# Performance work log

Measured on AMD Instinct MI355X. Metric: run time of the kernel, lower is better.

The kernel has to match this reference:

```python
import jax, jax.numpy as jnp
import numpy as np
from jax import lax

C_EDGE, C_DVS, C_OUT = 128, 128, 128
H, W = 32, 32
MASK_SIZE = 7
THRESH, TAU, GAMA = 1.0, 0.5, 1.0  # LIFSpike defaults (ZIF surrogate)


def _window_mask(h, w, mask_size):
    half = mask_size // 2
    qx = jnp.arange(h)[:, None, None, None]
    qy = jnp.arange(w)[None, :, None, None]
    kx = jnp.arange(h)[None, None, :, None]
    ky = jnp.arange(w)[None, None, None, :]
    allowed = (jnp.abs(kx - qx) <= half) & (jnp.abs(ky - qy) <= half)
    return jnp.where(allowed, 0.0, -10000.0).reshape(h * w, h * w).astype(jnp.float32)


@jax.custom_vjp
def _spike(x):
    return (x > 0).astype(x.dtype)

def _spike_fwd(x):
    return _spike(x), x

def _spike_bwd(x, g):
    # ZIF surrogate: grad = clamp(gama - |x|, 0) / gama^2
    return (g * jnp.clip(GAMA - jnp.abs(x), 0.0, None) / (GAMA * GAMA),)

_spike.defvjp(_spike_fwd, _spike_bwd)


def _lif(x):
    # x: (B, T, C, H, W) -> spikes, scan over time
    xt = jnp.moveaxis(x, 1, 0)  # (T, B, C, H, W)

    def step(mem, inp):
        mem = mem * TAU + inp
        spk = _spike(mem - THRESH)
        mem = (1.0 - spk) * mem
        return mem, spk

    _, spikes = lax.scan(step, jnp.zeros_like(xt[0]), xt)
    return jnp.moveaxis(spikes, 0, 1)


def setup_inputs() -> dict:
    key = jax.random.key(0)
    ks = jax.random.split(key, 16)
    s = 0.05
    return {
        "edge_features": jax.random.normal(ks[0], (8, 4, C_EDGE, H, W), jnp.float32),
        "dvs_features": jax.random.normal(ks[1], (8, 4, C_DVS, H, W), jnp.float32),
        "We": jax.random.normal(ks[2], (C_OUT, C_EDGE), jnp.float32) * s,
        "be": jax.random.normal(ks[3], (C_OUT,), jnp.float32) * s,
        "Wd": jax.random.normal(ks[4], (C_OUT, C_DVS), jnp.float32) * s,
        "bd": jax.random.normal(ks[5], (C_OUT,), jnp.float32) * s,
        "Wq": jax.random.normal(ks[6], (C_OUT, C_OUT), jnp.float32) * s,
        "bq": jax.random.normal(ks[7], (C_OUT,), jnp.float32) * s,
        "Wk": jax.random.normal(ks[8], (C_OUT, C_OUT), jnp.float32) * s,
        "bk": jax.random.normal(ks[9], (C_OUT,), jnp.float32) * s,
        "Wv": jax.random.normal(ks[10], (C_OUT, C_OUT), jnp.float32) * s,
        "bv": jax.random.normal(ks[11], (C_OUT,), jnp.float32) * s,
        "Wf": jax.random.normal(ks[12], (C_OUT, C_OUT), jnp.float32) * s,
        "bf": jax.random.normal(ks[13], (C_OUT,), jnp.float32) * s,
    }


def reference(edge_features, dvs_features, We, be, Wd, bd, Wq, bq, Wk, bk, Wv, bv, Wf, bf):
    B, T, _, h, w = dvs_features.shape
    C = We.shape[0]
    N = h * w
    # 1x1 conv channel alignment (SeqToANNContainer folds B,T)
    ef = (jnp.einsum('btchw,oc->btohw', edge_features, We) + be[None, None, :, None, None]).reshape(B * T, C, h, w)
    df = (jnp.einsum('btchw,oc->btohw', dvs_features, Wd) + bd[None, None, :, None, None]).reshape(B * T, C, h, w)
    # cosine similarity over channels
    l2e = jnp.sqrt(jnp.sum(ef * ef, axis=1, keepdims=True))
    l2d = jnp.sqrt(jnp.sum(df * df, axis=1, keepdims=True))
    sim = jnp.sum((ef / (l2e + 1e-6)) * (df / (l2d + 1e-6)), axis=1, keepdims=True)
    sim = (sim + 1.0) * 0.5
    # density: softmax of edge L2 norm over spatial, scaled by N
    dens = (jax.nn.softmax(l2e.reshape(B * T, N), axis=1) * N).reshape(B * T, 1, h, w)
    ew = (ef * sim).reshape(B * T, C, N)
    dw = (df * dens).reshape(B * T, C, N)
    # conv1d k=1 Q/K/V projections
    q = jnp.einsum('oc,bcn->bon', Wq, ew) + bq[None, :, None]
    k = jnp.einsum('oc,bcn->bon', Wk, dw) + bk[None, :, None]
    v = jnp.einsum('oc,bcn->bon', Wv, dw) + bv[None, :, None]
    mask = _window_mask(h, w, MASK_SIZE)
    attn = jnp.einsum('bcq,bck->bqk', q, k) / (C ** 0.5) + mask[None]
    attn = jax.nn.softmax(attn, axis=-1)
    out = jnp.einsum('bqk,bck->bqc', attn, v)  # (BT, N, C)
    out = out.reshape(B * T, h, w, C).transpose(0, 3, 1, 2).reshape(B, T, C, h, w)
    fused = jnp.einsum('btchw,oc->btohw', out, Wf) + bf[None, None, :, None, None]
    return _lif(fused)
```

## Files before the change

kernel.cpp:

```cpp
#include <hip/hip_runtime.h>
#include <math.h>

#define CC 128
#define NN 1024
#define BTOT 32
#define CP 152
#define PSTs 40
#define CPA 136
#define CQS 36

typedef unsigned short u16;
typedef u16 u16x8 __attribute__((ext_vector_type(8)));
typedef u16 u16x4 __attribute__((ext_vector_type(4)));
typedef __bf16 bf16x8 __attribute__((ext_vector_type(8)));
typedef float f32x4 __attribute__((ext_vector_type(4)));

__device__ __forceinline__ u16 f2b(float f) {
    unsigned int u = __float_as_uint(f);
    u += 0x7FFFu + ((u >> 16) & 1u);
    return (u16)(u >> 16);
}
__device__ __forceinline__ float b2f(u16 u) {
    return __uint_as_float(((unsigned int)u) << 16);
}

__device__ __forceinline__ void loadB(const u16* brow, int g, bf16x8 bfr[4]) {
#pragma unroll
    for (int kk = 0; kk < 4; ++kk)
        bfr[kk] = *(const bf16x8*)(brow + kk * 32 + g * 8);
}
__device__ __forceinline__ bf16x8 ldA(const u16* __restrict__ WB, int ot, int kk, int l) {
    return *(const bf16x8*)(WB + ((size_t)(ot * 4 + kk) * 64 + l) * 8);
}

__global__ __launch_bounds__(128) void k_comp(
    const float* __restrict__ Wq, const float* __restrict__ Wk,
    const float* __restrict__ Wv, const float* __restrict__ We,
    const float* __restrict__ Wd, const float* __restrict__ be,
    const float* __restrict__ bd,
    float* __restrict__ Wcomp, float* __restrict__ cvec)
{
    const int mat = blockIdx.y, o = blockIdx.x, c = threadIdx.x;
    const float* A = (mat == 0) ? Wq : (mat == 1) ? Wk : Wv;
    const float* B = (mat == 0) ? We : Wd;
    const float* bv = (mat == 0) ? be : bd;
    float acc = 0.f;
    for (int m = 0; m < CC; ++m) acc += A[o * CC + m] * B[m * CC + c];
    Wcomp[(size_t)mat * 16384 + o * CC + c] = acc;
    if (c == 0) {
        float bacc = 0.f;
        for (int m = 0; m < CC; ++m) bacc += A[o * CC + m] * bv[m];
        cvec[mat * CC + o] = bacc;
    }
}

__global__ __launch_bounds__(256) void k_wcvt(
    const float* __restrict__ W0, const float* __restrict__ W1,
    const float* __restrict__ W2, const float* __restrict__ W3,
    const float* __restrict__ W4, const float* __restrict__ W5,
    u16* __restrict__ out)
{
    const int gid = blockIdx.x * 256 + threadIdx.x;
    const int wi = gid >> 11, rem = gid & 2047;
    const float* W = (wi == 0) ? W0 : (wi == 1) ? W1 : (wi == 2) ? W2
                   : (wi == 3) ? W3 : (wi == 4) ? W4 : W5;
    const int ot = rem >> 8, kk = (rem >> 6) & 3, l = rem & 63;
    const int row = ot * 16 + (l & 15), col = kk * 32 + (l >> 4) * 8;
    float4 a = *(const float4*)(W + row * CC + col);
    float4 b = *(const float4*)(W + row * CC + col + 4);
    u16x8 u;
    u[0] = f2b(a.x); u[1] = f2b(a.y); u[2] = f2b(a.z); u[3] = f2b(a.w);
    u[4] = f2b(b.x); u[5] = f2b(b.y); u[6] = f2b(b.z); u[7] = f2b(b.w);
    *(u16x8*)(out + (size_t)wi * 16384 + ((size_t)(ot * 4 + kk) * 64 + l) * 8) = u;
}

__global__ __launch_bounds__(256) void k_front(
    const float* __restrict__ edge, const float* __restrict__ dvs,
    const u16* __restrict__ WeB, const u16* __restrict__ WdB,
    const u16* __restrict__ WqeB, const u16* __restrict__ WkdB,
    const u16* __restrict__ WvdB,
    const float* __restrict__ be, const float* __restrict__ bd,
    const float* __restrict__ bq,
    const float* __restrict__ cq, const float* __restrict__ ck,
    const float* __restrict__ cv,
    float* __restrict__ l2e_out,
    u16* __restrict__ qT, u16* __restrict__ kT, u16* __restrict__ vN)
{
    __shared__ u16 bufA[64 * CP];
    __shared__ u16 bufB[64 * CP];
    const int t = threadIdx.x;
    const int bt = blockIdx.y;
    const int n0b = blockIdx.x * 64;
    const float* eb = edge + (size_t)bt * CC * NN + n0b;
    const float* db = dvs + (size_t)bt * CC * NN + n0b;

#pragma unroll
    for (int j = 0; j < 2; ++j) {
        const int i = t + 256 * j;
        const int c4 = i >> 4, p = i & 15;
        float4 e[4], d[4];
#pragma unroll
        for (int m = 0; m < 4; ++m) {
            e[m] = *(const float4*)(eb + (size_t)(4 * c4 + m) * NN + 4 * p);
            d[m] = *(const float4*)(db + (size_t)(4 * c4 + m) * NN + 4 * p);
        }
#pragma unroll
        for (int n = 0; n < 4; ++n) {
            u16x4 ue, ud;
            ue[0] = f2b(((const float*)&e[0])[n]); ud[0] = f2b(((const float*)&d[0])[n]);
            ue[1] = f2b(((const float*)&e[1])[n]); ud[1] = f2b(((const float*)&d[1])[n]);
            ue[2] = f2b(((const float*)&e[2])[n]); ud[2] = f2b(((const float*)&d[2])[n]);
            ue[3] = f2b(((const float*)&e[3])[n]); ud[3] = f2b(((const float*)&d[3])[n]);
            *(u16x4*)&bufA[(4 * p + n) * CP + 4 * c4] = ue;
            *(u16x4*)&bufB[(4 * p + n) * CP + 4 * c4] = ud;
        }
    }
    __syncthreads();

    const int l = t & 63, w = t >> 6;
    const int l15 = l & 15, g = l >> 4;
    const int nloc = w * 16 + l15;
    const size_t gn = (size_t)bt * NN + n0b + nloc;

    bf16x8 bfrE[4], bfrD[4];
    loadB(bufA + nloc * CP, g, bfrE);
    loadB(bufB + nloc * CP, g, bfrD);

    f32x4 aE[8], aD[8];
#pragma unroll
    for (int ot = 0; ot < 8; ++ot) {
        aE[ot] = *(const f32x4*)(be + 16 * ot + 4 * g);
        aD[ot] = *(const f32x4*)(bd + 16 * ot + 4 * g);
    }
#pragma unroll
    for (int ot = 0; ot < 8; ++ot)
#pragma unroll
        for (int kk = 0; kk < 4; ++kk) {
            aE[ot] = __builtin_amdgcn_mfma_f32_16x16x32_bf16(ldA(WeB, ot, kk, l), bfrE[kk], aE[ot], 0, 0, 0);
            aD[ot] = __builtin_amdgcn_mfma_f32_16x16x32_bf16(ldA(WdB, ot, kk, l), bfrD[kk], aD[ot], 0, 0, 0);
        }
    float s2e = 0.f, s2d = 0.f, sed = 0.f;
#pragma unroll
    for (int ot = 0; ot < 8; ++ot)
#pragma unroll
        for (int r = 0; r < 4; ++r) {
            const float fe = aE[ot][r], fd = aD[ot][r];
            s2e += fe * fe; s2d += fd * fd; sed += fe * fd;
        }
    s2e += __shfl_xor(s2e, 16); s2e += __shfl_xor(s2e, 32);
    s2d += __shfl_xor(s2d, 16); s2d += __shfl_xor(s2d, 32);
    sed += __shfl_xor(sed, 16); sed += __shfl_xor(sed, 32);
    const float le = sqrtf(s2e), ld = sqrtf(s2d);
    const float sim = (sed / ((le + 1e-6f) * (ld + 1e-6f)) + 1.0f) * 0.5f;
    if (g == 0) l2e_out[gn] = le;

    {
        f32x4 aQ[8];
#pragma unroll
        for (int ot = 0; ot < 8; ++ot) aQ[ot] = *(const f32x4*)(cq + 16 * ot + 4 * g);
#pragma unroll
        for (int ot = 0; ot < 8; ++ot)
#pragma unroll
            for (int kk = 0; kk < 4; ++kk)
                aQ[ot] = __builtin_amdgcn_mfma_f32_16x16x32_bf16(ldA(WqeB, ot, kk, l), bfrE[kk], aQ[ot], 0, 0, 0);
#pragma unroll
        for (int ot = 0; ot < 8; ++ot) {
            f32x4 b4 = *(const f32x4*)(bq + 16 * ot + 4 * g);
            u16x4 u;
#pragma unroll
            for (int r = 0; r < 4; ++r) u[r] = f2b(sim * aQ[ot][r] + b4[r]);
            *(u16x4*)(qT + gn * CC + 16 * ot + 4 * g) = u;
        }
    }
    {
        f32x4 aK[8];
#pragma unroll
        for (int ot = 0; ot < 8; ++ot) aK[ot] = *(const f32x4*)(ck + 16 * ot + 4 * g);
#pragma unroll
        for (int ot = 0; ot < 8; ++ot)
#pragma unroll
            for (int kk = 0; kk < 4; ++kk)
                aK[ot] = __builtin_amdgcn_mfma_f32_16x16x32_bf16(ldA(WkdB, ot, kk, l), bfrD[kk], aK[ot], 0, 0, 0);
#pragma unroll
        for (int ot = 0; ot < 8; ++ot) {
            u16x4 u;
#pragma unroll
            for (int r = 0; r < 4; ++r) u[r] = f2b(aK[ot][r]);
            *(u16x4*)(kT + gn * CC + 16 * ot + 4 * g) = u;
        }
    }
    {
        f32x4 aV[8];
#pragma unroll
        for (int ot = 0; ot < 8; ++ot) aV[ot] = *(const f32x4*)(cv + 16 * ot + 4 * g);
#pragma unroll
        for (int ot = 0; ot < 8; ++ot)
#pragma unroll
            for (int kk = 0; kk < 4; ++kk)
                aV[ot] = __builtin_amdgcn_mfma_f32_16x16x32_bf16(ldA(WvdB, ot, kk, l), bfrD[kk], aV[ot], 0, 0, 0);
        __syncthreads();
        u16* bufT = bufA;
#pragma unroll
        for (int ot = 0; ot < 8; ++ot)
#pragma unroll
            for (int r = 0; r < 4; ++r)
                bufT[(16 * ot + 4 * g + r) * 72 + nloc] = f2b(aV[ot][r]);
        __syncthreads();
#pragma unroll
        for (int p = 0; p < 4; ++p) {
            const int idx = t + 256 * p;
            const int c = idx >> 3, n8 = (idx & 7) * 8;
            *(u16x8*)(vN + ((size_t)bt * CC + c) * NN + n0b + n8) =
                *(const u16x8*)&bufT[c * 72 + n8];
        }
    }
}

__global__ __launch_bounds__(256) void k_dens(const float* __restrict__ l2e,
                                              float* __restrict__ dens)
{
    __shared__ float red1[4];
    __shared__ float red2[4];
    const int bt = blockIdx.x, t = threadIdx.x;
    const int lane = t & 63, wid = t >> 6;
    const float* x = l2e + (size_t)bt * NN;
    float v[4], m = -1e30f;
#pragma unroll
    for (int i = 0; i < 4; ++i) { v[i] = x[t + 256 * i]; m = fmaxf(m, v[i]); }
#pragma unroll
    for (int off = 32; off >= 1; off >>= 1) m = fmaxf(m, __shfl_xor(m, off));
    if (lane == 0) red1[wid] = m;
    __syncthreads();
    m = fmaxf(fmaxf(red1[0], red1[1]), fmaxf(red1[2], red1[3]));
    float e[4], s = 0.f;
#pragma unroll
    for (int i = 0; i < 4; ++i) { e[i] = expf(v[i] - m); s += e[i]; }
#pragma unroll
    for (int off = 32; off >= 1; off >>= 1) s += __shfl_xor(s, off);
    if (lane == 0) red2[wid] = s;
    __syncthreads();
    s = red2[0] + red2[1] + red2[2] + red2[3];
    const float scale = 1024.0f / s;
#pragma unroll
    for (int i = 0; i < 4; ++i) dens[(size_t)bt * NN + t + 256 * i] = e[i] * scale;
}

__global__ __launch_bounds__(256) void k_attnf(
    const u16* __restrict__ qT, const u16* __restrict__ kT,
    const u16* __restrict__ vN, const float* __restrict__ dens,
    const float* __restrict__ bk, const float* __restrict__ bv,
    const u16* __restrict__ WfB, const float* __restrict__ bf,
    float* __restrict__ out)
{
    __shared__ u16 lds_u16[26624];
    const int t = threadIdx.x;
    const int id = blockIdx.x;
    const int b = id & 7, qx = id >> 3;
    const int w = t >> 6;
    const int bt = b * 4 + w;
    const int l = t & 63, l15 = l & 15, g = l >> 4;
    u16* att = lds_u16;
    float* convq = (float*)(lds_u16 + 17408);
    u16* P = lds_u16 + w * 32 * PSTs;
    const size_t btNN = (size_t)bt * NN;
    const float invsq = 0.08838834764831843f;

    u16x8 ql[2][4];
#pragma unroll
    for (int nt = 0; nt < 2; ++nt)
#pragma unroll
        for (int kk = 0; kk < 4; ++kk)
            ql[nt][kk] = *(const u16x8*)(qT + (btNN + qx * 32 + 16 * nt + l15) * CC + 32 * kk + 8 * g);

    float qbk[2] = {0.f, 0.f};
#pragma unroll
    for (int kk = 0; kk < 4; ++kk) {
        f32x4 b0 = *(const f32x4*)(bk + 32 * kk + 8 * g);
        f32x4 b1 = *(const f32x4*)(bk + 32 * kk + 8 * g + 4);
#pragma unroll
        for (int nt = 0; nt < 2; ++nt)
#pragma unroll
            for (int j = 0; j < 4; ++j) {
                qbk[nt] += b2f(ql[nt][kk][j]) * b0[j];
                qbk[nt] += b2f(ql[nt][kk][4 + j]) * b1[j];
            }
    }
#pragma unroll
    for (int nt = 0; nt < 2; ++nt) {
        qbk[nt] += __shfl_xor(qbk[nt], 16);
        qbk[nt] += __shfl_xor(qbk[nt], 32);
    }

    float ssum[2] = {0.f, 0.f};
    f32x4 o[8][2];
#pragma unroll
    for (int mt = 0; mt < 8; ++mt)
#pragma unroll
        for (int nt = 0; nt < 2; ++nt) o[mt][nt] = (f32x4){0.f, 0.f, 0.f, 0.f};

#pragma unroll
    for (int i = 0; i < 7; ++i) {
        const int kxr = qx - 3 + i;
        const int kxc = min(max(kxr, 0), 31);
        const bool cval = (kxr == kxc);
        f32x4 acc[2][2];
#pragma unroll
        for (int mt = 0; mt < 2; ++mt)
#pragma unroll
            for (int nt = 0; nt < 2; ++nt) acc[mt][nt] = (f32x4){0.f, 0.f, 0.f, 0.f};
#pragma unroll
        for (int kk = 0; kk < 4; ++kk)
#pragma unroll
            for (int mt = 0; mt < 2; ++mt) {
                bf16x8 ka = *(const bf16x8*)(kT + (btNN + kxc * 32 + 16 * mt + l15) * CC + 32 * kk + 8 * g);
#pragma unroll
                for (int nt = 0; nt < 2; ++nt)
                    acc[mt][nt] = __builtin_amdgcn_mfma_f32_16x16x32_bf16(
                        ka, __builtin_bit_cast(bf16x8, ql[nt][kk]), acc[mt][nt], 0, 0, 0);
            }
#pragma unroll
        for (int mt = 0; mt < 2; ++mt) {
            f32x4 d4 = *(const f32x4*)(dens + btNN + kxc * 32 + 16 * mt + 4 * g);
#pragma unroll
            for (int nt = 0; nt < 2; ++nt) {
                const int qyv = l15 + 16 * nt;
                u16x4 pw;
#pragma unroll
                for (int r = 0; r < 4; ++r) {
                    const float s = (d4[r] * acc[mt][nt][r] + qbk[nt]) * invsq;
                    const int ky = 16 * mt + 4 * g + r;
                    const int dy = ky - qyv;
                    const bool vld = cval && (dy >= -3) && (dy <= 3);
                    const float e = vld ? __expf(s) : 0.f;
                    ssum[nt] += e;
                    pw[r] = f2b(e * d4[r]);
                }
                *(u16x4*)&P[qyv * PSTs + 16 * mt + 4 * g] = pw;
            }
        }
        asm volatile("s_waitcnt lgkmcnt(0)" ::: "memory");
        __builtin_amdgcn_sched_barrier(0);
        bf16x8 pb[2];
#pragma unroll
        for (int nt = 0; nt < 2; ++nt)
            pb[nt] = *(const bf16x8*)&P[(16 * nt + l15) * PSTs + 8 * g];
#pragma unroll
        for (int mt = 0; mt < 8; ++mt) {
            bf16x8 va = *(const bf16x8*)(vN + ((size_t)bt * CC + 16 * mt + l15) * NN + kxc * 32 + 8 * g);
#pragma unroll
            for (int nt = 0; nt < 2; ++nt)
                o[mt][nt] = __builtin_amdgcn_mfma_f32_16x16x32_bf16(va, pb[nt], o[mt][nt], 0, 0, 0);
        }
    }
    float inv[2];
#pragma unroll
    for (int nt = 0; nt < 2; ++nt) {
        float s = ssum[nt];
        s += __shfl_xor(s, 16);
        s += __shfl_xor(s, 32);
        inv[nt] = 1.0f / s;
    }

    __syncthreads();

    u16* attw = att + w * 32 * CPA;
#pragma unroll
    for (int mt = 0; mt < 8; ++mt) {
        f32x4 bv4 = *(const f32x4*)(bv + 16 * mt + 4 * g);
#pragma unroll
        for (int nt = 0; nt < 2; ++nt) {
            u16x4 ov;
#pragma unroll
            for (int r = 0; r < 4; ++r) ov[r] = f2b(o[mt][nt][r] * inv[nt] + bv4[r]);
            *(u16x4*)&attw[(16 * nt + l15) * CPA + 16 * mt + 4 * g] = ov;
        }
    }
    asm volatile("s_waitcnt lgkmcnt(0)" ::: "memory");
    __builtin_amdgcn_sched_barrier(0);

    bf16x8 cb[4][2];
#pragma unroll
    for (int kk = 0; kk < 4; ++kk)
#pragma unroll
        for (int nt = 0; nt < 2; ++nt)
            cb[kk][nt] = *(const bf16x8*)&attw[(16 * nt + l15) * CPA + 32 * kk + 8 * g];

    const int cl = t >> 3, n4 = (t & 7) * 4;
#pragma unroll
    for (int cr = 0; cr < 4; ++cr) {
#pragma unroll
        for (int oi = 0; oi < 2; ++oi) {
            const int ot = 2 * cr + oi;
            f32x4 ca[2];
#pragma unroll
            for (int nt = 0; nt < 2; ++nt) ca[nt] = *(const f32x4*)(bf + 16 * ot + 4 * g);
#pragma unroll
            for (int kk = 0; kk < 4; ++kk) {
                bf16x8 afr = ldA(WfB, ot, kk, l);
#pragma unroll
                for (int nt = 0; nt < 2; ++nt)
                    ca[nt] = __builtin_amdgcn_mfma_f32_16x16x32_bf16(afr, cb[kk][nt], ca[nt], 0, 0, 0);
            }
#pragma unroll
            for (int nt = 0; nt < 2; ++nt)
#pragma unroll
                for (int r = 0; r < 4; ++r)
                    convq[w * 32 * CQS + (16 * oi + 4 * g + r) * CQS + 16 * nt + l15] = ca[nt][r];
        }
        __syncthreads();
        f32x4 mem = {0.f, 0.f, 0.f, 0.f};
#pragma unroll
        for (int tt = 0; tt < 4; ++tt) {
            f32x4 x = *(const f32x4*)&convq[tt * 32 * CQS + cl * CQS + n4];
            f32x4 mv = mem * 0.5f + x;
            float4 sp;
            sp.x = (mv[0] > 1.0f) ? 1.0f : 0.0f; if (mv[0] > 1.0f) mv[0] = 0.f;
            sp.y = (mv[1] > 1.0f) ? 1.0f : 0.0f; if (mv[1] > 1.0f) mv[1] = 0.f;
            sp.z = (mv[2] > 1.0f) ? 1.0f : 0.0f; if (mv[2] > 1.0f) mv[2] = 0.f;
            sp.w = (mv[3] > 1.0f) ? 1.0f : 0.0f; if (mv[3] > 1.0f) mv[3] = 0.f;
            *(float4*)(out + ((size_t)(b * 4 + tt) * CC + 32 * cr + cl) * NN + qx * 32 + n4) = sp;
            mem = mv;
        }
        __syncthreads();
    }
}

extern "C" void kernel_launch(void* const* d_in, const int* in_sizes, int n_in,
                              void* d_out, int out_size, void* d_ws, size_t ws_size,
                              hipStream_t stream) {
    (void)in_sizes; (void)n_in; (void)out_size; (void)ws_size;
    const float* edge = (const float*)d_in[0];
    const float* dvs  = (const float*)d_in[1];
    const float* We = (const float*)d_in[2];
    const float* be = (const float*)d_in[3];
    const float* Wd = (const float*)d_in[4];
    const float* bd = (const float*)d_in[5];
    const float* Wq = (const float*)d_in[6];
    const float* bq = (const float*)d_in[7];
    const float* Wk = (const float*)d_in[8];
    const float* bk = (const float*)d_in[9];
    const float* Wv = (const float*)d_in[10];
    const float* bv = (const float*)d_in[11];
    const float* Wf = (const float*)d_in[12];
    const float* bf = (const float*)d_in[13];
    float* out = (float*)d_out;

    const size_t S = (size_t)BTOT * NN * CC;
    u16* qT   = (u16*)d_ws;
    u16* kT   = qT + S;
    u16* vN   = kT + S;
    u16* WbAll = vN + S;
    float* fbase = (float*)(WbAll + 6 * 16384);
    float* Wcomp = fbase;
    float* cvec  = Wcomp + 3 * 16384;
    float* l2e   = cvec + 3 * CC;
    float* dens  = l2e + BTOT * NN;
    u16* WeB  = WbAll + 0 * 16384;
    u16* WdB  = WbAll + 1 * 16384;
    u16* WqeB = WbAll + 2 * 16384;
    u16* WkdB = WbAll + 3 * 16384;
    u16* WvdB = WbAll + 4 * 16384;
    u16* WfB  = WbAll + 5 * 16384;
    float* cq = cvec;
    float* ck = cvec + CC;
    float* cv = cvec + 2 * CC;

    k_comp<<<dim3(128, 3), 128, 0, stream>>>(Wq, Wk, Wv, We, Wd, be, bd, Wcomp, cvec);
    k_wcvt<<<48, 256, 0, stream>>>(We, Wd, Wcomp, Wcomp + 16384, Wcomp + 32768, Wf, WbAll);
    k_front<<<dim3(16, BTOT), 256, 0, stream>>>(edge, dvs, WeB, WdB, WqeB, WkdB, WvdB,
                                                be, bd, bq, cq, ck, cv, l2e, qT, kT, vN);
    k_dens<<<BTOT, 256, 0, stream>>>(l2e, dens);
    k_attnf<<<256, 256, 0, stream>>>(qT, kT, vN, dens, bk, bv, WfB, bf, out);
}
```

Baseline: 68.95 us.

## Merge weight prep kernels, halve front tiles with wave specialization, double attention waves

Fuses the weight-composition and bf16 conversion kernels into one launch that writes composed weights directly in MFMA layout. The front kernel now processes 32 positions per block (twice the blocks), with half the waves computing edge/Q/similarity and the other half computing K/V. The attention kernel uses 512 threads so each wave handles 16 query rows instead of 32, and the final conv/LIF stage is split across the extra waves. This raises parallelism and cuts a launch, at the cost of more blocks, extra barriers and duplicated weight loads.

```diff
diff --git a/kernel.cpp b/kernel.cpp
--- a/kernel.cpp
+++ b/kernel.cpp
@@ -33,45 +33,48 @@
     return *(const bf16x8*)(WB + ((size_t)(ot * 4 + kk) * 64 + l) * 8);
 }
 
-__global__ __launch_bounds__(128) void k_comp(
-    const float* __restrict__ Wq, const float* __restrict__ Wk,
-    const float* __restrict__ Wv, const float* __restrict__ We,
-    const float* __restrict__ Wd, const float* __restrict__ be,
-    const float* __restrict__ bd,
-    float* __restrict__ Wcomp, float* __restrict__ cvec)
+__global__ __launch_bounds__(256) void k_prep(
+    const float* __restrict__ We, const float* __restrict__ Wd,
+    const float* __restrict__ Wf, const float* __restrict__ Wq,
+    const float* __restrict__ Wk, const float* __restrict__ Wv,
+    const float* __restrict__ be, const float* __restrict__ bd,
+    u16* __restrict__ out, float* __restrict__ cvec)
 {
-    const int mat = blockIdx.y, o = blockIdx.x, c = threadIdx.x;
-    const float* A = (mat == 0) ? Wq : (mat == 1) ? Wk : Wv;
-    const float* B = (mat == 0) ? We : Wd;
-    const float* bv = (mat == 0) ? be : bd;
-    float acc = 0.f;
-    for (int m = 0; m < CC; ++m) acc += A[o * CC + m] * B[m * CC + c];
-    Wcomp[(size_t)mat * 16384 + o * CC + c] = acc;
-    if (c == 0) {
-        float bacc = 0.f;
-        for (int m = 0; m < CC; ++m) bacc += A[o * CC + m] * bv[m];
-        cvec[mat * CC + o] = bacc;
-    }
-}
-
-__global__ __launch_bounds__(256) void k_wcvt(
-    const float* __restrict__ W0, const float* __restrict__ W1,
-    const float* __restrict__ W2, const float* __restrict__ W3,
-    const float* __restrict__ W4, const float* __restrict__ W5,
-    u16* __restrict__ out)
-{
-    const int gid = blockIdx.x * 256 + threadIdx.x;
-    const int wi = gid >> 11, rem = gid & 2047;
-    const float* W = (wi == 0) ? W0 : (wi == 1) ? W1 : (wi == 2) ? W2
-                   : (wi == 3) ? W3 : (wi == 4) ? W4 : W5;
-    const int ot = rem >> 8, kk = (rem >> 6) & 3, l = rem & 63;
-    const int row = ot * 16 + (l & 15), col = kk * 32 + (l >> 4) * 8;
-    float4 a = *(const float4*)(W + row * CC + col);
-    float4 b = *(const float4*)(W + row * CC + col + 4);
-    u16x8 u;
-    u[0] = f2b(a.x); u[1] = f2b(a.y); u[2] = f2b(a.z); u[3] = f2b(a.w);
-    u[4] = f2b(b.x); u[5] = f2b(b.y); u[6] = f2b(b.z); u[7] = f2b(b.w);
-    *(u16x8*)(out + (size_t)wi * 16384 + ((size_t)(ot * 4 + kk) * 64 + l) * 8) = u;
+    const int bid = blockIdx.x, t = threadIdx.x;
+    if (bid < 24) {
+        const int gid = bid * 256 + t;
+        const int wi = gid >> 11;
+        const float* W = (wi == 0) ? We : (wi == 1) ? Wd : Wf;
+        const int slot = (wi == 2) ? 5 : wi;
+        const int rem = gid & 2047;
+        const int ot = rem >> 8, kk = (rem >> 6) & 3, l = rem & 63;
+        const int row = ot * 16 + (l & 15), col = kk * 32 + (l >> 4) * 8;
+        float4 a = *(const float4*)(W + row * CC + col);
+        float4 b = *(const float4*)(W + row * CC + col + 4);
+        u16x8 u;
+        u[0] = f2b(a.x); u[1] = f2b(a.y); u[2] = f2b(a.z); u[3] = f2b(a.w);
+        u[4] = f2b(b.x); u[5] = f2b(b.y); u[6] = f2b(b.z); u[7] = f2b(b.w);
+        *(u16x8*)(out + (size_t)slot * 16384 + ((size_t)(ot * 4 + kk) * 64 + l) * 8) = u;
+    } else {
+        const int cid = bid - 24;
+        const int mat = cid >> 6;
+        const int o = ((cid & 63) << 1) | (t >> 7);
+        const int c = t & 127;
+        const float* A = (mat == 0) ? Wq : (mat == 1) ? Wk : Wv;
+        const float* B = (mat == 0) ? We : Wd;
+        const float* bvec = (mat == 0) ? be : bd;
+        float acc = 0.f;
+        for (int m = 0; m < CC; ++m) acc += A[o * CC + m] * B[m * CC + c];
+        const int ot = o >> 4, l15o = o & 15;
+        const int kk = c >> 5, gc = (c >> 3) & 3, j = c & 7;
+        const int l = gc * 16 + l15o;
+        out[(size_t)(2 + mat) * 16384 + ((size_t)(ot * 4 + kk) * 64 + l) * 8 + j] = f2b(acc);
+        if (c == 0) {
+            float bacc = 0.f;
+            for (int m = 0; m < CC; ++m) bacc += A[o * CC + m] * bvec[m];
+            cvec[mat * CC + o] = bacc;
+        }
+    }
 }
 
 __global__ __launch_bounds__(256) void k_front(
@@ -86,18 +89,17 @@
     float* __restrict__ l2e_out,
     u16* __restrict__ qT, u16* __restrict__ kT, u16* __restrict__ vN)
 {
-    __shared__ u16 bufA[64 * CP];
-    __shared__ u16 bufB[64 * CP];
+    __shared__ u16 lds[2 * 32 * CP];
+    u16* bufA = lds;
+    u16* bufB = lds + 32 * CP;
     const int t = threadIdx.x;
     const int bt = blockIdx.y;
-    const int n0b = blockIdx.x * 64;
+    const int n0b = blockIdx.x * 32;
     const float* eb = edge + (size_t)bt * CC * NN + n0b;
     const float* db = dvs + (size_t)bt * CC * NN + n0b;
 
-#pragma unroll
-    for (int j = 0; j < 2; ++j) {
-        const int i = t + 256 * j;
-        const int c4 = i >> 4, p = i & 15;
+    {
+        const int c4 = t >> 3, p = t & 7;
         float4 e[4], d[4];
 #pragma unroll
         for (int m = 0; m < 4; ++m) {
@@ -117,44 +119,48 @@
     }
     __syncthreads();
 
-    const int l = t & 63, w = t >> 6;
+    const int w = t >> 6, l = t & 63;
     const int l15 = l & 15, g = l >> 4;
-    const int nloc = w * 16 + l15;
+    const bool is_e = (w < 2);
+    const int nloc = (w & 1) * 16 + l15;
     const size_t gn = (size_t)bt * NN + n0b + nloc;
 
     bf16x8 bfrE[4], bfrD[4];
-    loadB(bufA + nloc * CP, g, bfrE);
+    if (is_e) loadB(bufA + nloc * CP, g, bfrE);
     loadB(bufB + nloc * CP, g, bfrD);
-
-    f32x4 aE[8], aD[8];
-#pragma unroll
-    for (int ot = 0; ot < 8; ++ot) {
-        aE[ot] = *(const f32x4*)(be + 16 * ot + 4 * g);
-        aD[ot] = *(const f32x4*)(bd + 16 * ot + 4 * g);
-    }
-#pragma unroll
-    for (int ot = 0; ot < 8; ++ot)
-#pragma unroll
-        for (int kk = 0; kk < 4; ++kk) {
-            aE[ot] = __builtin_amdgcn_mfma_f32_16x16x32_bf16(ldA(WeB, ot, kk, l), bfrE[kk], aE[ot], 0, 0, 0);
-            aD[ot] = __builtin_amdgcn_mfma_f32_16x16x32_bf16(ldA(WdB, ot, kk, l), bfrD[kk], aD[ot], 0, 0, 0);
-        }
-    float s2e = 0.f, s2d = 0.f, sed = 0.f;
-#pragma unroll
-    for (int ot = 0; ot < 8; ++ot)
-#pragma unroll
-        for (int r = 0; r < 4; ++r) {
-            const float fe = aE[ot][r], fd = aD[ot][r];
-            s2e += fe * fe; s2d += fd * fd; sed += fe * fd;
-        }
-    s2e += __shfl_xor(s2e, 16); s2e += __shfl_xor(s2e, 32);
-    s2d += __shfl_xor(s2d, 16); s2d += __shfl_xor(s2d, 32);
-    sed += __shfl_xor(sed, 16); sed += __shfl_xor(sed, 32);
-    const float le = sqrtf(s2e), ld = sqrtf(s2d);
-    const float sim = (sed / ((le + 1e-6f) * (ld + 1e-6f)) + 1.0f) * 0.5f;
-    if (g == 0) l2e_out[gn] = le;
-
-    {
+    __syncthreads();
+
+    u16* bufT = lds;
+
+    if (is_e) {
+        f32x4 aE[8], aD[8];
+#pragma unroll
+        for (int ot = 0; ot < 8; ++ot) {
+            aE[ot] = *(const f32x4*)(be + 16 * ot + 4 * g);
+            aD[ot] = *(const f32x4*)(bd + 16 * ot + 4 * g);
+        }
+#pragma unroll
+        for (int ot = 0; ot < 8; ++ot)
+#pragma unroll
+            for (int kk = 0; kk < 4; ++kk) {
+                aE[ot] = __builtin_amdgcn_mfma_f32_16x16x32_bf16(ldA(WeB, ot, kk, l), bfrE[kk], aE[ot], 0, 0, 0);
+                aD[ot] = __builtin_amdgcn_mfma_f32_16x16x32_bf16(ldA(WdB, ot, kk, l), bfrD[kk], aD[ot], 0, 0, 0);
+            }
+        float s2e = 0.f, s2d = 0.f, sed = 0.f;
+#pragma unroll
+        for (int ot = 0; ot < 8; ++ot)
+#pragma unroll
+            for (int r = 0; r < 4; ++r) {
+                const float fe = aE[ot][r], fd = aD[ot][r];
+                s2e += fe * fe; s2d += fd * fd; sed += fe * fd;
+            }
+        s2e += __shfl_xor(s2e, 16); s2e += __shfl_xor(s2e, 32);
+        s2d += __shfl_xor(s2d, 16); s2d += __shfl_xor(s2d, 32);
+        sed += __shfl_xor(sed, 16); sed += __shfl_xor(sed, 32);
+        const float le = sqrtf(s2e), ld = sqrtf(s2d);
+        const float sim = (sed / ((le + 1e-6f) * (ld + 1e-6f)) + 1.0f) * 0.5f;
+        if (g == 0) l2e_out[gn] = le;
+
         f32x4 aQ[8];
 #pragma unroll
         for (int ot = 0; ot < 8; ++ot) aQ[ot] = *(const f32x4*)(cq + 16 * ot + 4 * g);
@@ -171,8 +177,7 @@
             for (int r = 0; r < 4; ++r) u[r] = f2b(sim * aQ[ot][r] + b4[r]);
             *(u16x4*)(qT + gn * CC + 16 * ot + 4 * g) = u;
         }
-    }
-    {
+    } else {
         f32x4 aK[8];
 #pragma unroll
         for (int ot = 0; ot < 8; ++ot) aK[ot] = *(const f32x4*)(ck + 16 * ot + 4 * g);
@@ -188,8 +193,6 @@
             for (int r = 0; r < 4; ++r) u[r] = f2b(aK[ot][r]);
             *(u16x4*)(kT + gn * CC + 16 * ot + 4 * g) = u;
         }
-    }
-    {
         f32x4 aV[8];
 #pragma unroll
         for (int ot = 0; ot < 8; ++ot) aV[ot] = *(const f32x4*)(cv + 16 * ot + 4 * g);
@@ -198,21 +201,19 @@
 #pragma unroll
             for (int kk = 0; kk < 4; ++kk)
                 aV[ot] = __builtin_amdgcn_mfma_f32_16x16x32_bf16(ldA(WvdB, ot, kk, l), bfrD[kk], aV[ot], 0, 0, 0);
-        __syncthreads();
-        u16* bufT = bufA;
 #pragma unroll
         for (int ot = 0; ot < 8; ++ot)
 #pragma unroll
             for (int r = 0; r < 4; ++r)
-                bufT[(16 * ot + 4 * g + r) * 72 + nloc] = f2b(aV[ot][r]);
-        __syncthreads();
-#pragma unroll
-        for (int p = 0; p < 4; ++p) {
-            const int idx = t + 256 * p;
-            const int c = idx >> 3, n8 = (idx & 7) * 8;
-            *(u16x8*)(vN + ((size_t)bt * CC + c) * NN + n0b + n8) =
-                *(const u16x8*)&bufT[c * 72 + n8];
-        }
+                bufT[(16 * ot + 4 * g + r) * 40 + nloc] = f2b(aV[ot][r]);
+    }
+    __syncthreads();
+#pragma unroll
+    for (int p = 0; p < 2; ++p) {
+        const int idx = t + 256 * p;
+        const int c = idx >> 2, n8 = (idx & 3) * 8;
+        *(u16x8*)(vN + ((size_t)bt * CC + c) * NN + n0b + n8) =
+            *(const u16x8*)&bufT[c * 40 + n8];
     }
 }
 
@@ -245,7 +246,7 @@
     for (int i = 0; i < 4; ++i) dens[(size_t)bt * NN + t + 256 * i] = e[i] * scale;
 }
 
-__global__ __launch_bounds__(256) void k_attnf(
+__global__ __launch_bounds__(512) void k_attnf(
     const u16* __restrict__ qT, const u16* __restrict__ kT,
     const u16* __restrict__ vN, const float* __restrict__ dens,
     const float* __restrict__ bk, const float* __restrict__ bv,
@@ -256,127 +257,98 @@
     const int t = threadIdx.x;
     const int id = blockIdx.x;
     const int b = id & 7, qx = id >> 3;
-    const int w = t >> 6;
-    const int bt = b * 4 + w;
+    const int w = t >> 6, tt = w & 3, h = w >> 2;
+    const int bt = b * 4 + tt;
     const int l = t & 63, l15 = l & 15, g = l >> 4;
     u16* att = lds_u16;
     float* convq = (float*)(lds_u16 + 17408);
-    u16* P = lds_u16 + w * 32 * PSTs;
+    u16* P = lds_u16 + tt * 32 * PSTs;
     const size_t btNN = (size_t)bt * NN;
     const float invsq = 0.08838834764831843f;
-
-    u16x8 ql[2][4];
-#pragma unroll
-    for (int nt = 0; nt < 2; ++nt)
-#pragma unroll
-        for (int kk = 0; kk < 4; ++kk)
-            ql[nt][kk] = *(const u16x8*)(qT + (btNN + qx * 32 + 16 * nt + l15) * CC + 32 * kk + 8 * g);
-
-    float qbk[2] = {0.f, 0.f};
+    const int qyv = 16 * h + l15;
+
+    u16x8 ql[4];
+#pragma unroll
+    for (int kk = 0; kk < 4; ++kk)
+        ql[kk] = *(const u16x8*)(qT + (btNN + qx * 32 + qyv) * CC + 32 * kk + 8 * g);
+
+    float qbk = 0.f;
 #pragma unroll
     for (int kk = 0; kk < 4; ++kk) {
         f32x4 b0 = *(const f32x4*)(bk + 32 * kk + 8 * g);
         f32x4 b1 = *(const f32x4*)(bk + 32 * kk + 8 * g + 4);
 #pragma unroll
-        for (int nt = 0; nt < 2; ++nt)
-#pragma unroll
-            for (int j = 0; j < 4; ++j) {
-                qbk[nt] += b2f(ql[nt][kk][j]) * b0[j];
-                qbk[nt] += b2f(ql[nt][kk][4 + j]) * b1[j];
-            }
-    }
-#pragma unroll
-    for (int nt = 0; nt < 2; ++nt) {
-        qbk[nt] += __shfl_xor(qbk[nt], 16);
-        qbk[nt] += __shfl_xor(qbk[nt], 32);
-    }
-
-    float ssum[2] = {0.f, 0.f};
-    f32x4 o[8][2];
-#pragma unroll
-    for (int mt = 0; mt < 8; ++mt)
-#pragma unroll
-        for (int nt = 0; nt < 2; ++nt) o[mt][nt] = (f32x4){0.f, 0.f, 0.f, 0.f};
+        for (int j = 0; j < 4; ++j) {
+            qbk += b2f(ql[kk][j]) * b0[j];
+            qbk += b2f(ql[kk][4 + j]) * b1[j];
+        }
+    }
+    qbk += __shfl_xor(qbk, 16);
+    qbk += __shfl_xor(qbk, 32);
+
+    float ssum = 0.f;
+    f32x4 o[8];
+#pragma unroll
+    for (int mt = 0; mt < 8; ++mt) o[mt] = (f32x4){0.f, 0.f, 0.f, 0.f};
 
 #pragma unroll
     for (int i = 0; i < 7; ++i) {
         const int kxr = qx - 3 + i;
         const int kxc = min(max(kxr, 0), 31);
         const bool cval = (kxr == kxc);
-        f32x4 acc[2][2];
-#pragma unroll
-        for (int mt = 0; mt < 2; ++mt)
-#pragma unroll
-            for (int nt = 0; nt < 2; ++nt) acc[mt][nt] = (f32x4){0.f, 0.f, 0.f, 0.f};
+        f32x4 acc[2];
+#pragma unroll
+        for (int mt = 0; mt < 2; ++mt) acc[mt] = (f32x4){0.f, 0.f, 0.f, 0.f};
 #pragma unroll
         for (int kk = 0; kk < 4; ++kk)
 #pragma unroll
             for (int mt = 0; mt < 2; ++mt) {
                 bf16x8 ka = *(const bf16x8*)(kT + (btNN + kxc * 32 + 16 * mt + l15) * CC + 32 * kk + 8 * g);
-#pragma unroll
-                for (int nt = 0; nt < 2; ++nt)
-                    acc[mt][nt] = __builtin_amdgcn_mfma_f32_16x16x32_bf16(
-                        ka, __builtin_bit_cast(bf16x8, ql[nt][kk]), acc[mt][nt], 0, 0, 0);
+                acc[mt] = __builtin_amdgcn_mfma_f32_16x16x32_bf16(
+                    ka, __builtin_bit_cast(bf16x8, ql[kk]), acc[mt], 0, 0, 0);
             }
 #pragma unroll
         for (int mt = 0; mt < 2; ++mt) {
             f32x4 d4 = *(const f32x4*)(dens + btNN + kxc * 32 + 16 * mt + 4 * g);
-#pragma unroll
-            for (int nt = 0; nt < 2; ++nt) {
-                const int qyv = l15 + 16 * nt;
-                u16x4 pw;
-#pragma unroll
-                for (int r = 0; r < 4; ++r) {
-                    const float s = (d4[r] * acc[mt][nt][r] + qbk[nt]) * invsq;
-                    const int ky = 16 * mt + 4 * g + r;
-                    const int dy = ky - qyv;
-                    const bool vld = cval && (dy >= -3) && (dy <= 3);
-                    const float e = vld ? __expf(s) : 0.f;
-                    ssum[nt] += e;
-                    pw[r] = f2b(e * d4[r]);
-                }
-                *(u16x4*)&P[qyv * PSTs + 16 * mt + 4 * g] = pw;
+            u16x4 pw;
+#pragma unroll
+            for (int r = 0; r < 4; ++r) {
+                const float s = (d4[r] * acc[mt][r] + qbk) * invsq;
+                const int ky = 16 * mt + 4 * g + r;
+                const int dy = ky - qyv;
+                const bool vld = cval && (dy >= -3) && (dy <= 3);
+                const float e = vld ? __expf(s) : 0.f;
+                ssum += e;
+                pw[r] = f2b(e * d4[r]);
             }
+            *(u16x4*)&P[qyv * PSTs + 16 * mt + 4 * g] = pw;
         }
         asm volatile("s_waitcnt lgkmcnt(0)" ::: "memory");
         __builtin_amdgcn_sched_barrier(0);
-        bf16x8 pb[2];
-#pragma unroll
-        for (int nt = 0; nt < 2; ++nt)
-            pb[nt] = *(const bf16x8*)&P[(16 * nt + l15) * PSTs + 8 * g];
+        bf16x8 pb = *(const bf16x8*)&P[qyv * PSTs + 8 * g];
 #pragma unroll
         for (int mt = 0; mt < 8; ++mt) {
             bf16x8 va = *(const bf16x8*)(vN + ((size_t)bt * CC + 16 * mt + l15) * NN + kxc * 32 + 8 * g);
-#pragma unroll
-            for (int nt = 0; nt < 2; ++nt)
-                o[mt][nt] = __builtin_amdgcn_mfma_f32_16x16x32_bf16(va, pb[nt], o[mt][nt], 0, 0, 0);
-        }
-    }
-    float inv[2];
-#pragma unroll
-    for (int nt = 0; nt < 2; ++nt) {
-        float s = ssum[nt];
-        s += __shfl_xor(s, 16);
-        s += __shfl_xor(s, 32);
-        inv[nt] = 1.0f / s;
-    }
-
-    __syncthreads();
-
-    u16* attw = att + w * 32 * CPA;
+            o[mt] = __builtin_amdgcn_mfma_f32_16x16x32_bf16(va, pb, o[mt], 0, 0, 0);
+        }
+    }
+    float s = ssum;
+    s += __shfl_xor(s, 16);
+    s += __shfl_xor(s, 32);
+    const float inv = 1.0f / s;
+
+    __syncthreads();
+
+    u16* attw = att + tt * 32 * CPA;
 #pragma unroll
     for (int mt = 0; mt < 8; ++mt) {
         f32x4 bv4 = *(const f32x4*)(bv + 16 * mt + 4 * g);
-#pragma unroll
-        for (int nt = 0; nt < 2; ++nt) {
-            u16x4 ov;
-#pragma unroll
-            for (int r = 0; r < 4; ++r) ov[r] = f2b(o[mt][nt][r] * inv[nt] + bv4[r]);
-            *(u16x4*)&attw[(16 * nt + l15) * CPA + 16 * mt + 4 * g] = ov;
-        }
-    }
-    asm volatile("s_waitcnt lgkmcnt(0)" ::: "memory");
-    __builtin_amdgcn_sched_barrier(0);
+        u16x4 ov;
+#pragma unroll
+        for (int r = 0; r < 4; ++r) ov[r] = f2b(o[mt][r] * inv + bv4[r]);
+        *(u16x4*)&attw[qyv * CPA + 16 * mt + 4 * g] = ov;
+    }
+    __syncthreads();
 
     bf16x8 cb[4][2];
 #pragma unroll
@@ -385,41 +357,36 @@
         for (int nt = 0; nt < 2; ++nt)
             cb[kk][nt] = *(const bf16x8*)&attw[(16 * nt + l15) * CPA + 32 * kk + 8 * g];
 
-    const int cl = t >> 3, n4 = (t & 7) * 4;
+    const int cl = t >> 4, n2 = (t & 15) * 2;
 #pragma unroll
     for (int cr = 0; cr < 4; ++cr) {
-#pragma unroll
-        for (int oi = 0; oi < 2; ++oi) {
-            const int ot = 2 * cr + oi;
-            f32x4 ca[2];
-#pragma unroll
-            for (int nt = 0; nt < 2; ++nt) ca[nt] = *(const f32x4*)(bf + 16 * ot + 4 * g);
-#pragma unroll
-            for (int kk = 0; kk < 4; ++kk) {
-                bf16x8 afr = ldA(WfB, ot, kk, l);
-#pragma unroll
-                for (int nt = 0; nt < 2; ++nt)
-                    ca[nt] = __builtin_amdgcn_mfma_f32_16x16x32_bf16(afr, cb[kk][nt], ca[nt], 0, 0, 0);
-            }
+        const int ot = 2 * cr + h;
+        f32x4 ca[2];
+#pragma unroll
+        for (int nt = 0; nt < 2; ++nt) ca[nt] = *(const f32x4*)(bf + 16 * ot + 4 * g);
+#pragma unroll
+        for (int kk = 0; kk < 4; ++kk) {
+            bf16x8 afr = ldA(WfB, ot, kk, l);
 #pragma unroll
             for (int nt = 0; nt < 2; ++nt)
-#pragma unroll
-                for (int r = 0; r < 4; ++r)
-                    convq[w * 32 * CQS + (16 * oi + 4 * g + r) * CQS + 16 * nt + l15] = ca[nt][r];
-        }
+                ca[nt] = __builtin_amdgcn_mfma_f32_16x16x32_bf16(afr, cb[kk][nt], ca[nt], 0, 0, 0);
+        }
+#pragma unroll
+        for (int nt = 0; nt < 2; ++nt)
+#pragma unroll
+            for (int r = 0; r < 4; ++r)
+                convq[tt * 32 * CQS + (16 * h + 4 * g + r) * CQS + 16 * nt + l15] = ca[nt][r];
         __syncthreads();
-        f32x4 mem = {0.f, 0.f, 0.f, 0.f};
-#pragma unroll
-        for (int tt = 0; tt < 4; ++tt) {
-            f32x4 x = *(const f32x4*)&convq[tt * 32 * CQS + cl * CQS + n4];
-            f32x4 mv = mem * 0.5f + x;
-            float4 sp;
-            sp.x = (mv[0] > 1.0f) ? 1.0f : 0.0f; if (mv[0] > 1.0f) mv[0] = 0.f;
-            sp.y = (mv[1] > 1.0f) ? 1.0f : 0.0f; if (mv[1] > 1.0f) mv[1] = 0.f;
-            sp.z = (mv[2] > 1.0f) ? 1.0f : 0.0f; if (mv[2] > 1.0f) mv[2] = 0.f;
-            sp.w = (mv[3] > 1.0f) ? 1.0f : 0.0f; if (mv[3] > 1.0f) mv[3] = 0.f;
-            *(float4*)(out + ((size_t)(b * 4 + tt) * CC + 32 * cr + cl) * NN + qx * 32 + n4) = sp;
-            mem = mv;
+        float m0 = 0.f, m1 = 0.f;
+#pragma unroll
+        for (int tt2 = 0; tt2 < 4; ++tt2) {
+            float2 x = *(const float2*)&convq[tt2 * 32 * CQS + cl * CQS + n2];
+            m0 = m0 * 0.5f + x.x;
+            m1 = m1 * 0.5f + x.y;
+            float2 sp;
+            sp.x = (m0 > 1.0f) ? 1.0f : 0.0f; if (m0 > 1.0f) m0 = 0.f;
+            sp.y = (m1 > 1.0f) ? 1.0f : 0.0f; if (m1 > 1.0f) m1 = 0.f;
+            *(float2*)(out + ((size_t)(b * 4 + tt2) * CC + 32 * cr + cl) * NN + qx * 32 + n2) = sp;
         }
         __syncthreads();
     }
@@ -451,8 +418,7 @@
     u16* vN   = kT + S;
     u16* WbAll = vN + S;
     float* fbase = (float*)(WbAll + 6 * 16384);
-    float* Wcomp = fbase;
-    float* cvec  = Wcomp + 3 * 16384;
+    float* cvec  = fbase;
     float* l2e   = cvec + 3 * CC;
     float* dens  = l2e + BTOT * NN;
     u16* WeB  = WbAll + 0 * 16384;
@@ -465,10 +431,9 @@
     float* ck = cvec + CC;
     float* cv = cvec + 2 * CC;
 
-    k_comp<<<dim3(128, 3), 128, 0, stream>>>(Wq, Wk, Wv, We, Wd, be, bd, Wcomp, cvec);
-    k_wcvt<<<48, 256, 0, stream>>>(We, Wd, Wcomp, Wcomp + 16384, Wcomp + 32768, Wf, WbAll);
-    k_front<<<dim3(16, BTOT), 256, 0, stream>>>(edge, dvs, WeB, WdB, WqeB, WkdB, WvdB,
+    k_prep<<<216, 256, 0, stream>>>(We, Wd, Wf, Wq, Wk, Wv, be, bd, WbAll, cvec);
+    k_front<<<dim3(32, BTOT), 256, 0, stream>>>(edge, dvs, WeB, WdB, WqeB, WkdB, WvdB,
                                                 be, bd, bq, cq, ck, cv, l2e, qT, kT, vN);
     k_dens<<<BTOT, 256, 0, stream>>>(l2e, dens);
-    k_attnf<<<256, 256, 0, stream>>>(qT, kT, vN, dens, bk, bv, WfB, bf, out);
-}
+    k_attnf<<<256, 512, 0, stream>>>(qT, kT, vN, dens, bk, bv, WfB, bf, out);
+}
```

New measurement: 78.89 us. 14.4% more time.
